# Performance work log

Measured on AMD Instinct MI355X. Metric: run time of the kernel, lower is better.

## Reference

```python
import jax, jax.numpy as jnp
import numpy as np

T, H, E = 1024, 2048, 32
I = 1024            # moe_intermediate_size
K = 8               # num_experts_per_token
G = 4               # num_expert_group
TOPK_GROUP = 2
N_SHARED = 2
IS = I * N_SHARED   # shared-expert intermediate
RSF = 2.5           # routed_scaling_factor


def setup_inputs() -> dict:
    key = jax.random.key(0)
    ks = jax.random.split(key, 9)
    s = 0.02
    return {
        "hidden_states": jax.random.normal(ks[0], (T, H), jnp.float32),
        "gate_w": jax.random.normal(ks[1], (H, E), jnp.float32) * s,
        "corr_bias": jax.random.normal(ks[2], (E,), jnp.float32) * s,
        "w_gate": jax.random.normal(ks[3], (E, H, I), jnp.float32) * s,
        "w_up": jax.random.normal(ks[4], (E, H, I), jnp.float32) * s,
        "w_down": jax.random.normal(ks[5], (E, I, H), jnp.float32) * s,
        "sw_gate": jax.random.normal(ks[6], (H, IS), jnp.float32) * s,
        "sw_up": jax.random.normal(ks[7], (H, IS), jnp.float32) * s,
        "sw_down": jax.random.normal(ks[8], (IS, H), jnp.float32) * s,
    }


def _route(x, gate_w, corr_bias):
    # biased grouped top-k (DeepSeek-V3 style sigmoid routing)
    logits = x @ gate_w                      # [T,E]
    scores = jax.nn.sigmoid(logits)
    sfc = scores + corr_bias[None, :]        # scores for choice
    grp = sfc.reshape(-1, G, E // G)
    # group score = sum of top-2 biased scores within the group
    grp_score = jax.lax.top_k(grp, 2)[0].sum(-1)          # [T,G]
    _, gidx = jax.lax.top_k(grp_score, TOPK_GROUP)        # [T,topk_group]
    rows = jnp.arange(sfc.shape[0])[:, None]
    gmask = jnp.zeros((sfc.shape[0], G), sfc.dtype).at[rows, gidx].set(1.0)
    emask = jnp.repeat(gmask, E // G, axis=1)             # [T,E]
    masked = jnp.where(emask > 0, sfc, -jnp.inf)
    _, idx = jax.lax.top_k(masked, K)                     # [T,K]
    w = jnp.take_along_axis(scores, idx, axis=1)          # unbiased scores
    w = w / w.sum(-1, keepdims=True)                      # renormalize
    w = w * RSF                                           # routed scaling
    combine = jnp.zeros((sfc.shape[0], E), x.dtype).at[rows, idx].add(w)
    return combine                                        # dense [T,E] combine weights


def reference(hidden_states, gate_w, corr_bias, w_gate, w_up, w_down,
              sw_gate, sw_up, sw_down):
    x = hidden_states
    # shared experts (SiLU-gated MLP)
    shared = (jax.nn.silu(x @ sw_gate) * (x @ sw_up)) @ sw_down   # [T,H]
    # routing
    combine = _route(x, gate_w, corr_bias)                        # [T,E]
    # routed experts (dense grouped-GEMM reference)
    g = jnp.einsum('th,ehi->tei', x, w_gate)
    u = jnp.einsum('th,ehi->tei', x, w_up)
    a = jax.nn.silu(g) * u                                        # [T,E,I]
    y = jnp.einsum('tei,eih->teh', a, w_down)                     # [T,E,H]
    routed = jnp.einsum('teh,te->th', y, combine)
    return routed + shared
```

## Files before the change

### kernel.cpp

```cpp
#include <hip/hip_runtime.h>

#define T_TOK 1024
#define H_DIM 2048
#define E_NUM 32
#define I_DIM 1024
#define IS_DIM 2048

typedef float  f32x4 __attribute__((ext_vector_type(4)));
typedef short  s16x8 __attribute__((ext_vector_type(8)));
typedef unsigned short u16x4 __attribute__((ext_vector_type(4)));
typedef unsigned short u16x8 __attribute__((ext_vector_type(8)));

__device__ __forceinline__ unsigned short f2bf(float f) {
    unsigned u = __builtin_bit_cast(unsigned, f);
    u = (u + 0x7fffu + ((u >> 16) & 1u)) >> 16;
    return (unsigned short)u;
}

__device__ __forceinline__ int swz(int r, int c) {
    return (r << 5) + (c ^ (((r >> 2) & 3) << 3));
}

__global__ __launch_bounds__(256) void cvt_k(
    const float* __restrict__ x, unsigned short* __restrict__ xb)
{
    const int i = (blockIdx.x * 256 + threadIdx.x) * 8;
    f32x4 a = *(const f32x4*)(x + i);
    f32x4 b = *(const f32x4*)(x + i + 4);
    u16x8 h = { f2bf(a[0]), f2bf(a[1]), f2bf(a[2]), f2bf(a[3]),
                f2bf(b[0]), f2bf(b[1]), f2bf(b[2]), f2bf(b[3]) };
    *(u16x8*)(xb + i) = h;
}

__global__ __launch_bounds__(256) void route_k(
    const float* __restrict__ x, const float* __restrict__ gw,
    const float* __restrict__ bias, int* __restrict__ tidx,
    float* __restrict__ tw)
{
    const int w = threadIdx.x >> 6;
    const int lane = threadIdx.x & 63;
    const int t = blockIdx.x * 4 + w;
    __shared__ float xs[4][H_DIM];
    __shared__ float sfc[4][E_NUM];
    __shared__ float sc[4][E_NUM];

    for (int i = threadIdx.x; i < 4 * (H_DIM / 4); i += 256) {
        int tt = i >> 9;
        int c = i & 511;
        *(f32x4*)&xs[tt][c * 4] =
            *(const f32x4*)(x + (size_t)(blockIdx.x * 4 + tt) * H_DIM + c * 4);
    }
    __syncthreads();

    const int eq = (lane & 7) * 4;
    const int hs = lane >> 3;
    f32x4 acc = {0.f, 0.f, 0.f, 0.f};
    #pragma unroll 4
    for (int h = hs; h < H_DIM; h += 8) {
        float xv = xs[w][h];
        f32x4 gv = *(const f32x4*)(gw + (size_t)h * E_NUM + eq);
        acc += gv * xv;
    }
    #pragma unroll
    for (int m = 8; m < 64; m <<= 1) {
        acc[0] += __shfl_xor(acc[0], m);
        acc[1] += __shfl_xor(acc[1], m);
        acc[2] += __shfl_xor(acc[2], m);
        acc[3] += __shfl_xor(acc[3], m);
    }
    if (lane < 8) {
        #pragma unroll
        for (int j = 0; j < 4; ++j) {
            float s = 1.f / (1.f + expf(-acc[j]));
            sc[w][eq + j] = s;
            sfc[w][eq + j] = s + bias[eq + j];
        }
    }
    __syncthreads();

    if (lane == 0) {
        float gs[4];
        for (int gg = 0; gg < 4; ++gg) {
            float m1 = -1e30f, m2 = -1e30f;
            for (int j = 0; j < 8; ++j) {
                float v = sfc[w][gg * 8 + j];
                if (v > m1) { m2 = m1; m1 = v; }
                else if (v > m2) { m2 = v; }
            }
            gs[gg] = m1 + m2;
        }
        int g1 = 0;
        for (int gg = 1; gg < 4; ++gg) if (gs[gg] > gs[g1]) g1 = gg;
        int g2 = (g1 == 0) ? 1 : 0;
        for (int gg = 0; gg < 4; ++gg)
            if (gg != g1 && gs[gg] > gs[g2]) g2 = gg;

        unsigned allow = (0xFFu << (g1 * 8)) | (0xFFu << (g2 * 8));
        unsigned taken = 0u;
        int   isel[8];
        float wsel[8];
        float wsum = 0.f;
        for (int k = 0; k < 8; ++k) {
            int best = 0; float bv = -1e30f;
            for (int e2 = 0; e2 < 32; ++e2) {
                if (((allow >> e2) & 1u) && !((taken >> e2) & 1u)) {
                    float v = sfc[w][e2];
                    if (v > bv) { bv = v; best = e2; }
                }
            }
            taken |= 1u << best;
            isel[k] = best;
            wsel[k] = sc[w][best];
            wsum += sc[w][best];
        }
        const float f = 2.5f / wsum;
        for (int k = 0; k < 8; ++k) {
            tidx[t * 8 + k] = isel[k];
            tw[t * 8 + k] = wsel[k] * f;
        }
    }
}

__global__ __launch_bounds__(64) void build_k(
    const int* __restrict__ tidx, const float* __restrict__ tw,
    int* __restrict__ ltok, float* __restrict__ lw, int* __restrict__ counts)
{
    const int e = blockIdx.x;
    const int lane = threadIdx.x;
    int cnt = 0;
    for (int t0 = 0; t0 < T_TOK; t0 += 64) {
        const int t = t0 + lane;
        int sel = 0; float w = 0.f;
        #pragma unroll
        for (int k = 0; k < 8; ++k) {
            if (tidx[t * 8 + k] == e) { sel = 1; w = tw[t * 8 + k]; }
        }
        unsigned long long m = __ballot(sel);
        int pos = __popcll(m & ((1ull << lane) - 1ull));
        if (sel) {
            ltok[e * T_TOK + cnt + pos] = t;
            lw[e * T_TOK + cnt + pos] = w;
        }
        cnt += __popcll(m);
    }
    if (lane == 0) counts[e] = cnt;
}

__global__ void prefix_k(const int* __restrict__ counts, int* __restrict__ offsets)
{
    if (threadIdx.x == 0) {
        int off = 0;
        for (int e = 0; e < E_NUM; ++e) { offsets[e] = off; off += counts[e]; }
    }
}

template<int DUAL, int EXPERT, int GATHER, int ATOMIC>
__global__ __launch_bounds__(256) void gemm_k(
    const unsigned short* __restrict__ A, const float* __restrict__ B1g,
    const float* __restrict__ B2g, void* __restrict__ outv,
    const int* __restrict__ counts, const int* __restrict__ offsets,
    const int* __restrict__ ltok, const float* __restrict__ lw,
    int M, int N, int K)
{
    constexpr int BM = 128;
    constexpr int WR = 32;
    constexpr int FM = 2;
    constexpr int NB = 2;

    const int e = blockIdx.z;
    const int Mloc = EXPERT ? counts[e] : M;
    const int col0 = blockIdx.y * 32;
    const int rb = EXPERT ? offsets[e] : 0;

    const float* B1 = B1g;
    const float* B2 = B2g;
    if (EXPERT) {
        size_t eo = (size_t)e * K * N;
        B1 += eo;
        if (DUAL) B2 += eo;
    }

    __shared__ unsigned short lA[2][BM * 32];
    __shared__ unsigned short lB[2][DUAL + 1][32 * 32];

    const int tid = threadIdx.x;
    const int lane = tid & 63;
    const int wv = tid >> 6;

    const int arow = tid >> 1;
    const int akb  = (tid & 1) * 16;

    const bool doB = tid < (DUAL ? 128 : 64);
    const int bmat = DUAL ? (tid >> 6) : 0;
    const int t6 = tid & 63;
    const int nq = t6 & 7;
    const int kq = t6 >> 3;
    const float* bp = (bmat ? B2 : B1) + (size_t)(4 * kq) * N + col0 + nq * 4;

    f32x4 acc1[FM][2], acc2[FM][2];
    u16x8 pbaX[NB], pbaY[NB];
    f32x4 pbX[4], pbY[4];
    const unsigned short* apb = nullptr;

    auto loadT = [&](int k0, u16x8 (&pba)[NB], f32x4 (&pb)[4]) {
        #pragma unroll
        for (int i = 0; i < NB; ++i)
            pba[i] = *(const u16x8*)(apb + k0 + i * 8);
        if (doB) {
            #pragma unroll
            for (int j = 0; j < 4; ++j)
                pb[j] = *(const f32x4*)(bp + (size_t)(k0 + j) * N);
        }
    };

    auto storeT = [&](int p, u16x8 (&pba)[NB], f32x4 (&pb)[4]) {
        #pragma unroll
        for (int i = 0; i < NB; ++i)
            *(u16x8*)&lA[p][swz(arow, akb + i * 8)] = pba[i];
        if (doB) {
            #pragma unroll
            for (int j2 = 0; j2 < 4; ++j2) {
                u16x4 h = { f2bf(pb[0][j2]), f2bf(pb[1][j2]),
                            f2bf(pb[2][j2]), f2bf(pb[3][j2]) };
                *(u16x4*)&lB[p][bmat][swz(nq * 4 + j2, kq * 4)] = h;
            }
        }
    };

    auto compute = [&](int p) {
        const int koff = (lane >> 4) * 8;
        s16x8 af[FM], b1f[2], b2f[2];
        #pragma unroll
        for (int fm = 0; fm < FM; ++fm)
            af[fm] = *(const s16x8*)&lA[p][swz(wv * WR + fm * 16 + (lane & 15), koff)];
        #pragma unroll
        for (int fn = 0; fn < 2; ++fn) {
            b1f[fn] = *(const s16x8*)&lB[p][0][swz(fn * 16 + (lane & 15), koff)];
            if (DUAL)
                b2f[fn] = *(const s16x8*)&lB[p][1][swz(fn * 16 + (lane & 15), koff)];
        }
        #pragma unroll
        for (int fm = 0; fm < FM; ++fm)
            #pragma unroll
            for (int fn = 0; fn < 2; ++fn) {
                acc1[fm][fn] = __builtin_amdgcn_mfma_f32_16x16x32_bf16(
                    af[fm], b1f[fn], acc1[fm][fn], 0, 0, 0);
                if (DUAL)
                    acc2[fm][fn] = __builtin_amdgcn_mfma_f32_16x16x32_bf16(
                        af[fm], b2f[fn], acc2[fm][fn], 0, 0, 0);
            }
    };

    const int nk = K >> 5;

    for (int row0 = blockIdx.x * BM; row0 < Mloc; row0 += gridDim.x * BM) {
        {
            int rr = row0 + arow;
            if (rr >= Mloc) rr = Mloc - 1;
            int grow = GATHER ? ltok[e * T_TOK + rr] : (rb + rr);
            apb = A + (size_t)grow * K + akb;
        }
        #pragma unroll
        for (int a = 0; a < FM; ++a)
            #pragma unroll
            for (int b = 0; b < 2; ++b) {
                acc1[a][b] = f32x4{0.f, 0.f, 0.f, 0.f};
                acc2[a][b] = f32x4{0.f, 0.f, 0.f, 0.f};
            }

        loadT(0, pbaX, pbX);
        loadT(32, pbaY, pbY);
        __syncthreads();
        storeT(0, pbaX, pbX);
        __syncthreads();

        for (int kt = 0; kt < nk; kt += 2) {
            if (kt + 2 < nk) loadT((kt + 2) << 5, pbaX, pbX);
            compute(0);
            storeT(1, pbaY, pbY);
            __syncthreads();
            if (kt + 3 < nk) loadT((kt + 3) << 5, pbaY, pbY);
            compute(1);
            if (kt + 2 < nk) {
                storeT(0, pbaX, pbX);
                __syncthreads();
            }
        }

        const int fr = (lane >> 4) << 2;
        const int fc = lane & 15;
        if (DUAL) {
            unsigned short* outp = (unsigned short*)outv;
            #pragma unroll
            for (int fm = 0; fm < FM; ++fm)
                #pragma unroll
                for (int fn = 0; fn < 2; ++fn)
                    #pragma unroll
                    for (int j = 0; j < 4; ++j) {
                        int r = wv * WR + fm * 16 + fr + j;
                        if (row0 + r < Mloc) {
                            int cc = col0 + fn * 16 + fc;
                            float gv = acc1[fm][fn][j];
                            float uv = acc2[fm][fn][j];
                            float a = gv / (1.f + expf(-gv)) * uv;
                            outp[(size_t)(rb + row0 + r) * N + cc] = f2bf(a);
                        }
                    }
        } else if (ATOMIC) {
            float* outp = (float*)outv;
            #pragma unroll
            for (int fm = 0; fm < FM; ++fm)
                #pragma unroll
                for (int fn = 0; fn < 2; ++fn)
                    #pragma unroll
                    for (int j = 0; j < 4; ++j) {
                        int r = wv * WR + fm * 16 + fr + j;
                        if (row0 + r < Mloc) {
                            int tok = ltok[e * T_TOK + row0 + r];
                            float wr = lw[e * T_TOK + row0 + r];
                            int cc = col0 + fn * 16 + fc;
                            atomicAdd(outp + (size_t)tok * N + cc, acc1[fm][fn][j] * wr);
                        }
                    }
        } else {
            float* outp = (float*)outv;
            #pragma unroll
            for (int fm = 0; fm < FM; ++fm)
                #pragma unroll
                for (int fn = 0; fn < 2; ++fn)
                    #pragma unroll
                    for (int j = 0; j < 4; ++j) {
                        int r = wv * WR + fm * 16 + fr + j;
                        if (row0 + r < Mloc) {
                            int cc = col0 + fn * 16 + fc;
                            outp[(size_t)(row0 + r) * N + cc] = acc1[fm][fn][j];
                        }
                    }
        }
    }
}

extern "C" void kernel_launch(void* const* d_in, const int* in_sizes, int n_in,
                              void* d_out, int out_size, void* d_ws, size_t ws_size,
                              hipStream_t stream) {
    const float* x       = (const float*)d_in[0];
    const float* gate_w  = (const float*)d_in[1];
    const float* bias    = (const float*)d_in[2];
    const float* w_gate  = (const float*)d_in[3];
    const float* w_up    = (const float*)d_in[4];
    const float* w_down  = (const float*)d_in[5];
    const float* sw_gate = (const float*)d_in[6];
    const float* sw_up   = (const float*)d_in[7];
    const float* sw_down = (const float*)d_in[8];
    float* out = (float*)d_out;

    char* ws = (char*)d_ws;
    int*   topk_idx = (int*)ws;
    float* topk_w   = (float*)(ws + 32768);
    int*   counts   = (int*)(ws + 65536);
    int*   offsets  = (int*)(ws + 65536 + 128);
    int*   ltok     = (int*)(ws + 65536 + 256);
    float* lw       = (float*)(ws + 65536 + 256 + 131072);
    unsigned short* act_s = (unsigned short*)(ws + 65536 + 256 + 262144);
    unsigned short* act_r = act_s + (size_t)T_TOK * IS_DIM;
    unsigned short* xbf   = act_r + (size_t)T_TOK * 8 * I_DIM;

    cvt_k<<<T_TOK * H_DIM / 2048, 256, 0, stream>>>(x, xbf);
    route_k<<<T_TOK / 4, 256, 0, stream>>>(x, gate_w, bias, topk_idx, topk_w);
    build_k<<<E_NUM, 64, 0, stream>>>(topk_idx, topk_w, ltok, lw, counts);
    prefix_k<<<1, 64, 0, stream>>>(counts, offsets);

    gemm_k<1,0,0,0><<<dim3(8, IS_DIM / 32, 1), 256, 0, stream>>>(
        xbf, sw_gate, sw_up, act_s, nullptr, nullptr, nullptr, nullptr,
        T_TOK, IS_DIM, H_DIM);
    gemm_k<1,1,1,0><<<dim3(1, I_DIM / 32, E_NUM), 256, 0, stream>>>(
        xbf, w_gate, w_up, act_r, counts, offsets, ltok, lw,
        T_TOK, I_DIM, H_DIM);
    gemm_k<0,0,0,0><<<dim3(8, H_DIM / 32, 1), 256, 0, stream>>>(
        act_s, sw_down, nullptr, out, nullptr, nullptr, nullptr, nullptr,
        T_TOK, H_DIM, IS_DIM);
    gemm_k<0,1,0,1><<<dim3(1, H_DIM / 32, E_NUM), 256, 0, stream>>>(
        act_r, w_down, nullptr, out, counts, offsets, ltok, lw,
        T_TOK, H_DIM, I_DIM);
}
```

Measured before the change: 783.2 us.

## Template GEMM row tile, use 256-row tiles for experts, single-stage prefetch

Makes the GEMM row-tile size a template parameter and uses 256-row tiles for the routed-expert GEMMs, so each block reads its expert weights fewer times across token row tiles. The two-deep register prefetch is reduced to a one-deep prefetch, and launch bounds now request 4 blocks per SM, both to cut register pressure. The larger tile doubles the A tile in LDS and the accumulators per wave, which can hurt occupancy. The shallower prefetch may also expose more global-load latency.

```diff
diff --git a/kernel.cpp b/kernel.cpp
--- a/kernel.cpp
+++ b/kernel.cpp
@@ -154,18 +154,19 @@
     }
 }
 
-template<int DUAL, int EXPERT, int GATHER, int ATOMIC>
-__global__ __launch_bounds__(256) void gemm_k(
+template<int DUAL, int EXPERT, int GATHER, int ATOMIC, int BM>
+__global__ __launch_bounds__(256, 4) void gemm_k(
     const unsigned short* __restrict__ A, const float* __restrict__ B1g,
     const float* __restrict__ B2g, void* __restrict__ outv,
     const int* __restrict__ counts, const int* __restrict__ offsets,
     const int* __restrict__ ltok, const float* __restrict__ lw,
     int M, int N, int K)
 {
-    constexpr int BM = 128;
-    constexpr int WR = 32;
-    constexpr int FM = 2;
-    constexpr int NB = 2;
+    constexpr int WR  = BM / 4;
+    constexpr int FM  = WR / 16;
+    constexpr int TPR = 256 / BM;
+    constexpr int KSP = 32 / TPR;
+    constexpr int NB  = KSP / 8;
 
     const int e = blockIdx.z;
     const int Mloc = EXPERT ? counts[e] : M;
@@ -187,8 +188,8 @@
     const int lane = tid & 63;
     const int wv = tid >> 6;
 
-    const int arow = tid >> 1;
-    const int akb  = (tid & 1) * 16;
+    const int arow = tid / TPR;
+    const int akb  = (tid % TPR) * KSP;
 
     const bool doB = tid < (DUAL ? 128 : 64);
     const int bmat = DUAL ? (tid >> 6) : 0;
@@ -198,11 +199,11 @@
     const float* bp = (bmat ? B2 : B1) + (size_t)(4 * kq) * N + col0 + nq * 4;
 
     f32x4 acc1[FM][2], acc2[FM][2];
-    u16x8 pbaX[NB], pbaY[NB];
-    f32x4 pbX[4], pbY[4];
+    u16x8 pba[NB];
+    f32x4 pb[4];
     const unsigned short* apb = nullptr;
 
-    auto loadT = [&](int k0, u16x8 (&pba)[NB], f32x4 (&pb)[4]) {
+    auto loadT = [&](int k0) {
         #pragma unroll
         for (int i = 0; i < NB; ++i)
             pba[i] = *(const u16x8*)(apb + k0 + i * 8);
@@ -213,7 +214,7 @@
         }
     };
 
-    auto storeT = [&](int p, u16x8 (&pba)[NB], f32x4 (&pb)[4]) {
+    auto storeT = [&](int p) {
         #pragma unroll
         for (int i = 0; i < NB; ++i)
             *(u16x8*)&lA[p][swz(arow, akb + i * 8)] = pba[i];
@@ -268,21 +269,16 @@
                 acc2[a][b] = f32x4{0.f, 0.f, 0.f, 0.f};
             }
 
-        loadT(0, pbaX, pbX);
-        loadT(32, pbaY, pbY);
+        loadT(0);
         __syncthreads();
-        storeT(0, pbaX, pbX);
+        storeT(0);
         __syncthreads();
 
-        for (int kt = 0; kt < nk; kt += 2) {
-            if (kt + 2 < nk) loadT((kt + 2) << 5, pbaX, pbX);
-            compute(0);
-            storeT(1, pbaY, pbY);
-            __syncthreads();
-            if (kt + 3 < nk) loadT((kt + 3) << 5, pbaY, pbY);
-            compute(1);
-            if (kt + 2 < nk) {
-                storeT(0, pbaX, pbX);
+        for (int kt = 0; kt < nk; ++kt) {
+            if (kt + 1 < nk) loadT((kt + 1) << 5);
+            compute(kt & 1);
+            if (kt + 1 < nk) {
+                storeT((kt + 1) & 1);
                 __syncthreads();
             }
         }
@@ -370,16 +366,16 @@
     build_k<<<E_NUM, 64, 0, stream>>>(topk_idx, topk_w, ltok, lw, counts);
     prefix_k<<<1, 64, 0, stream>>>(counts, offsets);
 
-    gemm_k<1,0,0,0><<<dim3(8, IS_DIM / 32, 1), 256, 0, stream>>>(
+    gemm_k<1,0,0,0,128><<<dim3(8, IS_DIM / 32, 1), 256, 0, stream>>>(
         xbf, sw_gate, sw_up, act_s, nullptr, nullptr, nullptr, nullptr,
         T_TOK, IS_DIM, H_DIM);
-    gemm_k<1,1,1,0><<<dim3(1, I_DIM / 32, E_NUM), 256, 0, stream>>>(
+    gemm_k<1,1,1,0,256><<<dim3(1, I_DIM / 32, E_NUM), 256, 0, stream>>>(
         xbf, w_gate, w_up, act_r, counts, offsets, ltok, lw,
         T_TOK, I_DIM, H_DIM);
-    gemm_k<0,0,0,0><<<dim3(8, H_DIM / 32, 1), 256, 0, stream>>>(
+    gemm_k<0,0,0,0,128><<<dim3(8, H_DIM / 32, 1), 256, 0, stream>>>(
         act_s, sw_down, nullptr, out, nullptr, nullptr, nullptr, nullptr,
         T_TOK, H_DIM, IS_DIM);
-    gemm_k<0,1,0,1><<<dim3(1, H_DIM / 32, E_NUM), 256, 0, stream>>>(
+    gemm_k<0,1,0,1,256><<<dim3(1, H_DIM / 32, E_NUM), 256, 0, stream>>>(
         act_r, w_down, nullptr, out, counts, offsets, ltok, lw,
         T_TOK, H_DIM, I_DIM);
 }
```

New measurement: 944.8 us. 20.6% more time.

## Split dual gate/up GEMMs into separate panels, add split-K for routed down GEMM

Applied to the files above, without the earlier changes.

The fused gate/up GEMM is split so each block computes only one of the two matrices, which doubles the grid in y and halves accumulator registers. The SiLU*up product moves into a separate elementwise kernel working on bf16 intermediates. The routed down-projection uses split-K of 2 with atomic accumulation, and launch bounds request 6 blocks per SM. Together these are meant to raise occupancy and parallelism for the small per-expert M. The cost is extra global traffic for the separate gate and up buffers, two extra kernel launches, bf16 rounding of gate and up before SiLU, and more atomics.

```diff
diff --git a/kernel.cpp b/kernel.cpp
--- a/kernel.cpp
+++ b/kernel.cpp
@@ -15,6 +15,9 @@
     unsigned u = __builtin_bit_cast(unsigned, f);
     u = (u + 0x7fffu + ((u >> 16) & 1u)) >> 16;
     return (unsigned short)u;
+}
+__device__ __forceinline__ float bf2f(unsigned short h) {
+    return __builtin_bit_cast(float, (unsigned)h << 16);
 }
 
 __device__ __forceinline__ int swz(int r, int c) {
@@ -30,6 +33,23 @@
     u16x8 h = { f2bf(a[0]), f2bf(a[1]), f2bf(a[2]), f2bf(a[3]),
                 f2bf(b[0]), f2bf(b[1]), f2bf(b[2]), f2bf(b[3]) };
     *(u16x8*)(xb + i) = h;
+}
+
+__global__ __launch_bounds__(256) void silu_k(
+    const unsigned short* __restrict__ g, const unsigned short* __restrict__ u,
+    unsigned short* __restrict__ o)
+{
+    const int i = (blockIdx.x * 256 + threadIdx.x) * 8;
+    u16x8 gv = *(const u16x8*)(g + i);
+    u16x8 uv = *(const u16x8*)(u + i);
+    u16x8 r;
+    #pragma unroll
+    for (int j = 0; j < 8; ++j) {
+        float gf = bf2f(gv[j]);
+        float uf = bf2f(uv[j]);
+        r[j] = f2bf(gf / (1.f + expf(-gf)) * uf);
+    }
+    *(u16x8*)(o + i) = r;
 }
 
 __global__ __launch_bounds__(256) void route_k(
@@ -154,10 +174,11 @@
     }
 }
 
-template<int DUAL, int EXPERT, int GATHER, int ATOMIC>
-__global__ __launch_bounds__(256) void gemm_k(
-    const unsigned short* __restrict__ A, const float* __restrict__ B1g,
-    const float* __restrict__ B2g, void* __restrict__ outv,
+template<int MSPLIT, int EXPERT, int GATHER, int OUTMODE, int KSPLIT>
+__global__ __launch_bounds__(256, 6) void gemm_k(
+    const unsigned short* __restrict__ A,
+    const float* __restrict__ B1g, const float* __restrict__ B2g,
+    void* __restrict__ out1v, void* __restrict__ out2v,
     const int* __restrict__ counts, const int* __restrict__ offsets,
     const int* __restrict__ ltok, const float* __restrict__ lw,
     int M, int N, int K)
@@ -169,19 +190,26 @@
 
     const int e = blockIdx.z;
     const int Mloc = EXPERT ? counts[e] : M;
-    const int col0 = blockIdx.y * 32;
     const int rb = EXPERT ? offsets[e] : 0;
 
-    const float* B1 = B1g;
-    const float* B2 = B2g;
-    if (EXPERT) {
-        size_t eo = (size_t)e * K * N;
-        B1 += eo;
-        if (DUAL) B2 += eo;
-    }
+    int ymat = 0, ypanel = blockIdx.y;
+    if (MSPLIT) {
+        const int half = gridDim.y >> 1;
+        ymat = (blockIdx.y >= half) ? 1 : 0;
+        ypanel = blockIdx.y - ymat * half;
+    }
+    const int col0 = ypanel * 32;
+    const float* B = ymat ? B2g : B1g;
+    void* outv = ymat ? out2v : out1v;
+    if (EXPERT) B += (size_t)e * K * N;
+
+    const int kbase = (KSPLIT > 1) ? blockIdx.x * (K / KSPLIT) : 0;
+    const int nk = (K / KSPLIT) >> 5;
+    const int m0 = (KSPLIT > 1) ? 0 : blockIdx.x * BM;
+    const int mstep = ((KSPLIT > 1) ? 1 : gridDim.x) * BM;
 
     __shared__ unsigned short lA[2][BM * 32];
-    __shared__ unsigned short lB[2][DUAL + 1][32 * 32];
+    __shared__ unsigned short lB[2][32 * 32];
 
     const int tid = threadIdx.x;
     const int lane = tid & 63;
@@ -190,14 +218,12 @@
     const int arow = tid >> 1;
     const int akb  = (tid & 1) * 16;
 
-    const bool doB = tid < (DUAL ? 128 : 64);
-    const int bmat = DUAL ? (tid >> 6) : 0;
-    const int t6 = tid & 63;
-    const int nq = t6 & 7;
-    const int kq = t6 >> 3;
-    const float* bp = (bmat ? B2 : B1) + (size_t)(4 * kq) * N + col0 + nq * 4;
-
-    f32x4 acc1[FM][2], acc2[FM][2];
+    const bool doB = tid < 64;
+    const int nq = tid & 7;
+    const int kq = (tid >> 3) & 7;
+    const float* bp = B + (size_t)(kbase + 4 * kq) * N + col0 + nq * 4;
+
+    f32x4 acc1[FM][2];
     u16x8 pbaX[NB], pbaY[NB];
     f32x4 pbX[4], pbY[4];
     const unsigned short* apb = nullptr;
@@ -222,51 +248,40 @@
             for (int j2 = 0; j2 < 4; ++j2) {
                 u16x4 h = { f2bf(pb[0][j2]), f2bf(pb[1][j2]),
                             f2bf(pb[2][j2]), f2bf(pb[3][j2]) };
-                *(u16x4*)&lB[p][bmat][swz(nq * 4 + j2, kq * 4)] = h;
+                *(u16x4*)&lB[p][swz(nq * 4 + j2, kq * 4)] = h;
             }
         }
     };
 
     auto compute = [&](int p) {
         const int koff = (lane >> 4) * 8;
-        s16x8 af[FM], b1f[2], b2f[2];
+        s16x8 af[FM], bf[2];
         #pragma unroll
         for (int fm = 0; fm < FM; ++fm)
             af[fm] = *(const s16x8*)&lA[p][swz(wv * WR + fm * 16 + (lane & 15), koff)];
         #pragma unroll
-        for (int fn = 0; fn < 2; ++fn) {
-            b1f[fn] = *(const s16x8*)&lB[p][0][swz(fn * 16 + (lane & 15), koff)];
-            if (DUAL)
-                b2f[fn] = *(const s16x8*)&lB[p][1][swz(fn * 16 + (lane & 15), koff)];
-        }
+        for (int fn = 0; fn < 2; ++fn)
+            bf[fn] = *(const s16x8*)&lB[p][swz(fn * 16 + (lane & 15), koff)];
         #pragma unroll
         for (int fm = 0; fm < FM; ++fm)
             #pragma unroll
-            for (int fn = 0; fn < 2; ++fn) {
+            for (int fn = 0; fn < 2; ++fn)
                 acc1[fm][fn] = __builtin_amdgcn_mfma_f32_16x16x32_bf16(
-                    af[fm], b1f[fn], acc1[fm][fn], 0, 0, 0);
-                if (DUAL)
-                    acc2[fm][fn] = __builtin_amdgcn_mfma_f32_16x16x32_bf16(
-                        af[fm], b2f[fn], acc2[fm][fn], 0, 0, 0);
-            }
+                    af[fm], bf[fn], acc1[fm][fn], 0, 0, 0);
     };
 
-    const int nk = K >> 5;
-
-    for (int row0 = blockIdx.x * BM; row0 < Mloc; row0 += gridDim.x * BM) {
+    for (int row0 = m0; row0 < Mloc; row0 += mstep) {
         {
             int rr = row0 + arow;
             if (rr >= Mloc) rr = Mloc - 1;
             int grow = GATHER ? ltok[e * T_TOK + rr] : (rb + rr);
-            apb = A + (size_t)grow * K + akb;
+            apb = A + (size_t)grow * K + kbase + akb;
         }
         #pragma unroll
         for (int a = 0; a < FM; ++a)
             #pragma unroll
-            for (int b = 0; b < 2; ++b) {
+            for (int b = 0; b < 2; ++b)
                 acc1[a][b] = f32x4{0.f, 0.f, 0.f, 0.f};
-                acc2[a][b] = f32x4{0.f, 0.f, 0.f, 0.f};
-            }
 
         loadT(0, pbaX, pbX);
         loadT(32, pbaY, pbY);
@@ -289,7 +304,7 @@
 
         const int fr = (lane >> 4) << 2;
         const int fc = lane & 15;
-        if (DUAL) {
+        if (OUTMODE == 0) {
             unsigned short* outp = (unsigned short*)outv;
             #pragma unroll
             for (int fm = 0; fm < FM; ++fm)
@@ -300,13 +315,24 @@
                         int r = wv * WR + fm * 16 + fr + j;
                         if (row0 + r < Mloc) {
                             int cc = col0 + fn * 16 + fc;
-                            float gv = acc1[fm][fn][j];
-                            float uv = acc2[fm][fn][j];
-                            float a = gv / (1.f + expf(-gv)) * uv;
-                            outp[(size_t)(rb + row0 + r) * N + cc] = f2bf(a);
+                            outp[(size_t)(rb + row0 + r) * N + cc] = f2bf(acc1[fm][fn][j]);
                         }
                     }
-        } else if (ATOMIC) {
+        } else if (OUTMODE == 1) {
+            float* outp = (float*)outv;
+            #pragma unroll
+            for (int fm = 0; fm < FM; ++fm)
+                #pragma unroll
+                for (int fn = 0; fn < 2; ++fn)
+                    #pragma unroll
+                    for (int j = 0; j < 4; ++j) {
+                        int r = wv * WR + fm * 16 + fr + j;
+                        if (row0 + r < Mloc) {
+                            int cc = col0 + fn * 16 + fc;
+                            outp[(size_t)(row0 + r) * N + cc] = acc1[fm][fn][j];
+                        }
+                    }
+        } else {
             float* outp = (float*)outv;
             #pragma unroll
             for (int fm = 0; fm < FM; ++fm)
@@ -322,20 +348,6 @@
                             atomicAdd(outp + (size_t)tok * N + cc, acc1[fm][fn][j] * wr);
                         }
                     }
-        } else {
-            float* outp = (float*)outv;
-            #pragma unroll
-            for (int fm = 0; fm < FM; ++fm)
-                #pragma unroll
-                for (int fn = 0; fn < 2; ++fn)
-                    #pragma unroll
-                    for (int j = 0; j < 4; ++j) {
-                        int r = wv * WR + fm * 16 + fr + j;
-                        if (row0 + r < Mloc) {
-                            int cc = col0 + fn * 16 + fc;
-                            outp[(size_t)(row0 + r) * N + cc] = acc1[fm][fn][j];
-                        }
-                    }
         }
     }
 }
@@ -361,25 +373,32 @@
     int*   offsets  = (int*)(ws + 65536 + 128);
     int*   ltok     = (int*)(ws + 65536 + 256);
     float* lw       = (float*)(ws + 65536 + 256 + 131072);
-    unsigned short* act_s = (unsigned short*)(ws + 65536 + 256 + 262144);
-    unsigned short* act_r = act_s + (size_t)T_TOK * IS_DIM;
-    unsigned short* xbf   = act_r + (size_t)T_TOK * 8 * I_DIM;
+    unsigned short* xbf = (unsigned short*)(ws + 65536 + 256 + 262144);
+    unsigned short* g_s = xbf + (size_t)T_TOK * H_DIM;
+    unsigned short* u_s = g_s + (size_t)T_TOK * IS_DIM;
+    unsigned short* g_r = u_s + (size_t)T_TOK * IS_DIM;
+    unsigned short* u_r = g_r + (size_t)T_TOK * 8 * I_DIM;
 
     cvt_k<<<T_TOK * H_DIM / 2048, 256, 0, stream>>>(x, xbf);
     route_k<<<T_TOK / 4, 256, 0, stream>>>(x, gate_w, bias, topk_idx, topk_w);
     build_k<<<E_NUM, 64, 0, stream>>>(topk_idx, topk_w, ltok, lw, counts);
     prefix_k<<<1, 64, 0, stream>>>(counts, offsets);
 
-    gemm_k<1,0,0,0><<<dim3(8, IS_DIM / 32, 1), 256, 0, stream>>>(
-        xbf, sw_gate, sw_up, act_s, nullptr, nullptr, nullptr, nullptr,
+    gemm_k<1,0,0,0,1><<<dim3(8, 128, 1), 256, 0, stream>>>(
+        xbf, sw_gate, sw_up, g_s, u_s, nullptr, nullptr, nullptr, nullptr,
         T_TOK, IS_DIM, H_DIM);
-    gemm_k<1,1,1,0><<<dim3(1, I_DIM / 32, E_NUM), 256, 0, stream>>>(
-        xbf, w_gate, w_up, act_r, counts, offsets, ltok, lw,
+    silu_k<<<T_TOK * IS_DIM / 2048, 256, 0, stream>>>(g_s, u_s, g_s);
+
+    gemm_k<1,1,1,0,1><<<dim3(1, 64, E_NUM), 256, 0, stream>>>(
+        xbf, w_gate, w_up, g_r, u_r, counts, offsets, ltok, lw,
         T_TOK, I_DIM, H_DIM);
-    gemm_k<0,0,0,0><<<dim3(8, H_DIM / 32, 1), 256, 0, stream>>>(
-        act_s, sw_down, nullptr, out, nullptr, nullptr, nullptr, nullptr,
+    silu_k<<<T_TOK * 8 * I_DIM / 2048, 256, 0, stream>>>(g_r, u_r, g_r);
+
+    gemm_k<0,0,0,1,1><<<dim3(8, 64, 1), 256, 0, stream>>>(
+        g_s, sw_down, nullptr, out, nullptr, nullptr, nullptr, nullptr, nullptr,
         T_TOK, H_DIM, IS_DIM);
-    gemm_k<0,1,0,1><<<dim3(1, H_DIM / 32, E_NUM), 256, 0, stream>>>(
-        act_r, w_down, nullptr, out, counts, offsets, ltok, lw,
+
+    gemm_k<0,1,0,2,2><<<dim3(2, 64, E_NUM), 256, 0, stream>>>(
+        g_r, w_down, nullptr, out, nullptr, counts, offsets, ltok, lw,
         T_TOK, H_DIM, I_DIM);
 }
```

Measured after the change: 2.219 ms. +183.3%, slower.
